# Kernel optimization log

Measured on AMD Instinct MI355X. Metric: run time of the kernel, lower is better.

The kernel has to match this reference:

```python
import jax, jax.numpy as jnp
import numpy as np

B, Nres, TOP_K, NUM_RBF = 2, 2048, 30, 16
MAX_REL = 32  # positional clip range -> 2*32+2 = 66 classes


def _gather_nodes(nodes, idx):
    # nodes: [B, N, ...], idx: [B, N, K] -> [B, N, K, ...]
    return jax.vmap(lambda n, i: n[i])(nodes, idx)


def _rbf(D):
    # D: [..., ] -> [..., NUM_RBF]; mu in [2, 22], sigma = 20/16
    mu = jnp.linspace(2.0, 22.0, NUM_RBF)
    sigma = (22.0 - 2.0) / NUM_RBF
    return jnp.exp(-(((D[..., None] - mu) / sigma) ** 2))


def setup_inputs() -> dict:
    key = jax.random.key(0)
    ks = jax.random.split(key, 4)
    X = jax.random.normal(ks[0], (B, Nres, 4, 3), dtype=jnp.float32) * 3.0
    mask = jnp.ones((B, Nres), dtype=jnp.float32)
    residue_idx = jnp.broadcast_to(jnp.arange(Nres, dtype=jnp.int32)[None], (B, Nres))
    chain_labels = jnp.zeros((B, Nres), dtype=jnp.int32)
    w_pos = jax.random.normal(ks[1], (66, 16), dtype=jnp.float32) * 0.05
    b_pos = jax.random.normal(ks[2], (16,), dtype=jnp.float32) * 0.05
    w_edge = jax.random.normal(ks[3], (416, 128), dtype=jnp.float32) * 0.05
    ln_gamma = jnp.ones((128,), dtype=jnp.float32)
    ln_beta = jnp.zeros((128,), dtype=jnp.float32)
    return dict(X=X, mask=mask, residue_idx=residue_idx, chain_labels=chain_labels,
                w_pos=w_pos, b_pos=b_pos, w_edge=w_edge, ln_gamma=ln_gamma, ln_beta=ln_beta)


def reference(X, mask, residue_idx, chain_labels, w_pos, b_pos, w_edge, ln_gamma, ln_beta):
    # virtual C-beta from N, C, Ca (atom order in X: N=0, C=1, Ca=2, O=3)
    b = X[:, :, 2, :] - X[:, :, 0, :]
    c = X[:, :, 1, :] - X[:, :, 2, :]
    a = jnp.cross(b, c)
    Cb = -0.58273431 * a + 0.56802827 * b - 0.54067466 * c + X[:, :, 2, :]
    N_, C, Ca, O = X[:, :, 0, :], X[:, :, 1, :], X[:, :, 2, :], X[:, :, 3, :]

    # masked kNN on C atoms (ProteinFeatures._dist)
    m2 = mask[:, None, :] * mask[:, :, None]                       # [B,N,N]
    dX = C[:, None, :, :] - C[:, :, None, :]
    D = m2 * jnp.sqrt(jnp.sum(dX ** 2, -1) + 1e-6)
    D_max = jnp.max(D, -1, keepdims=True)
    D_adj = D + (1.0 - m2) * D_max
    neg, E_idx = jax.lax.top_k(-D_adj, TOP_K)                      # smallest-k
    D_neighbors = -neg                                             # [B,N,K]

    # 25-channel RBF features; gather neighbor coords instead of NxN per pair
    atoms = jnp.stack([N_, Ca, Cb, C, O], 0)                       # [5,B,N,3]
    gathered = jax.vmap(lambda A: _gather_nodes(A, E_idx))(atoms)  # [5,B,N,K,3]
    # pair order follows torch source: NN,CaCa,CbCb,CN,CCa,CCb,NCa,NCb,CbCa,
    # NC,CaC,CbC,CaN,CbN,CaCb,OO,CO,OC,NO,ON,CbO,OCa,OCb,CaO  (0=N,1=Ca,2=Cb,3=C,4=O)
    pa = jnp.array([0, 1, 2, 3, 3, 3, 0, 0, 2, 0, 1, 2, 1, 2, 1, 4, 3, 4, 0, 4, 2, 4, 4, 1])
    pb = jnp.array([0, 1, 2, 0, 1, 2, 1, 2, 1, 3, 3, 3, 0, 0, 2, 4, 4, 3, 4, 0, 4, 1, 2, 4])
    A_sel = atoms[pa]                                              # [24,B,N,3]
    Bn_sel = gathered[pb]                                          # [24,B,N,K,3]
    Dp = jnp.sqrt(jnp.sum((A_sel[:, :, :, None, :] - Bn_sel) ** 2, -1) + 1e-6)
    RBF_all = jnp.concatenate([_rbf(D_neighbors)[None], _rbf(Dp)], 0)  # [25,B,N,K,16]
    RBF_all = jnp.moveaxis(RBF_all, 0, 3).reshape(B, Nres, TOP_K, 25 * NUM_RBF)

    # positional encodings over gathered offsets / chain match
    offset = residue_idx[:, :, None] - _gather_nodes(residue_idx, E_idx)   # [B,N,K]
    E_chains = (chain_labels[:, :, None] == _gather_nodes(chain_labels, E_idx)).astype(jnp.int32)
    d = jnp.clip(offset + MAX_REL, 0, 2 * MAX_REL) * E_chains + (1 - E_chains) * (2 * MAX_REL + 1)
    E_pos = w_pos[d] + b_pos                                       # one_hot @ W == gather

    # edge embedding + layernorm
    E = jnp.concatenate([E_pos, RBF_all], -1) @ w_edge             # [B,N,K,128]
    mu = E.mean(-1, keepdims=True)
    var = E.var(-1, keepdims=True)
    E = (E - mu) / jnp.sqrt(var + 1e-5) * ln_gamma + ln_beta
    return E, E_idx
```

## Files before the change

### kernel.cpp

```cpp
#include <hip/hip_runtime.h>
#include <hip/hip_bf16.h>
#include <stdint.h>

#define BB    2
#define NRES  2048
#define TOPK  30
#define NRBF  16
#define NFEAT 416
#define NCH   128
#define NSTR  212
#define NKT   13

typedef __attribute__((ext_vector_type(8))) short bf16x8;
typedef __attribute__((ext_vector_type(4))) float f32x4;

__constant__ int c_pa[24] = {0,1,2,3,3,3,0,0,2,0,1,2,1,2,1,4,3,4,0,4,2,4,4,1};
__constant__ int c_pb[24] = {0,1,2,0,1,2,1,2,1,3,3,3,0,0,2,4,4,3,4,0,4,1,2,4};

static __device__ __forceinline__ unsigned short f2bf(float x) {
  __hip_bfloat16 h = __float2bfloat16(x);
  return *reinterpret_cast<unsigned short*>(&h);
}
static __device__ __forceinline__ unsigned pack2(float lo, float hi) {
  return (unsigned)f2bf(lo) | ((unsigned)f2bf(hi) << 16);
}

__global__ __launch_bounds__(256) void atoms_kernel(const float* __restrict__ X,
                                                    float* __restrict__ atoms,
                                                    float4* __restrict__ Cpk) {
  int id = blockIdx.x * 256 + threadIdx.x;
  if (id >= BB * NRES) return;
  const float* x = X + (size_t)id * 12;
  float nx = x[0], ny = x[1], nz = x[2];
  float cx = x[3], cy = x[4], cz = x[5];
  float ax = x[6], ay = x[7], az = x[8];
  float ox = x[9], oy = x[10], oz = x[11];
  float bx = ax - nx, by = ay - ny, bz = az - nz;
  float ccx = cx - ax, ccy = cy - ay, ccz = cz - az;
  float crx = by * ccz - bz * ccy;
  float cry = bz * ccx - bx * ccz;
  float crz = bx * ccy - by * ccx;
  float cbx = -0.58273431f * crx + 0.56802827f * bx - 0.54067466f * ccx + ax;
  float cby = -0.58273431f * cry + 0.56802827f * by - 0.54067466f * ccy + ay;
  float cbz = -0.58273431f * crz + 0.56802827f * bz - 0.54067466f * ccz + az;
  float* r = atoms + (size_t)id * 16;
  r[0] = nx;  r[1] = ny;  r[2] = nz;
  r[3] = ax;  r[4] = ay;  r[5] = az;
  r[6] = cbx; r[7] = cby; r[8] = cbz;
  r[9] = cx;  r[10] = cy; r[11] = cz;
  r[12] = ox; r[13] = oy; r[14] = oz;
  r[15] = 0.f;
  Cpk[id] = make_float4(cx, cy, cz, 0.f);
}

__global__ __launch_bounds__(256) void wprep_kernel(const float* __restrict__ w_edge,
                                                    unsigned short* __restrict__ wB) {
  int id = blockIdx.x * 256 + threadIdx.x;
  if (id >= NFEAT * NCH) return;
  int j    = id & 7;
  int lane = (id >> 3) & 63;
  int nt   = (id >> 9) & 7;
  int kt   = id >> 12;
  int col  = nt * 16 + (lane & 15);
  int k    = kt * 32 + ((lane >> 4) << 3) + j;
  wB[id] = f2bf(w_edge[(size_t)k * NCH + col]);
}

__global__ __launch_bounds__(256) void topk_kernel(const float4* __restrict__ Cpk,
                                                   int* __restrict__ eidx,
                                                   float* __restrict__ dn,
                                                   float* __restrict__ outI) {
  int tid = threadIdx.x;
  int lane = tid & 63;
  int bi = blockIdx.x * 4 + (tid >> 6);
  int b = bi >> 11;
  int i = bi & (NRES - 1);
  const float4* Cb = Cpk + (size_t)b * NRES;
  float4 ci = Cb[i];

  unsigned long long key[4][8];
  unsigned long long sub[4];
#pragma unroll
  for (int g = 0; g < 4; ++g) {
    sub[g] = ~0ull;
#pragma unroll
    for (int s = 0; s < 8; ++s) {
      int j = lane + 64 * (g * 8 + s);
      float4 cj = Cb[j];
      float dx = cj.x - ci.x, dy = cj.y - ci.y, dz = cj.z - ci.z;
      float sm = __fadd_rn(__fadd_rn(__fadd_rn(__fmul_rn(dx, dx), __fmul_rn(dy, dy)),
                                     __fmul_rn(dz, dz)), 1e-6f);
      float d = sqrtf(sm);
      key[g][s] = ((unsigned long long)__float_as_uint(d) << 32) | (unsigned)j;
      if (key[g][s] < sub[g]) sub[g] = key[g][s];
    }
  }

  for (int k = 0; k < TOPK; ++k) {
    unsigned long long m01 = sub[0] < sub[1] ? sub[0] : sub[1];
    unsigned long long m23 = sub[2] < sub[3] ? sub[2] : sub[3];
    unsigned long long gm = m01 < m23 ? m01 : m23;
#pragma unroll
    for (int off = 32; off; off >>= 1) {
      unsigned long long o = __shfl_xor(gm, off, 64);
      if (o < gm) gm = o;
    }
    if (lane == 0) {
      int idx = (int)(unsigned)(gm & 0xffffffffu);
      eidx[(size_t)bi * TOPK + k] = idx;
      dn[(size_t)bi * TOPK + k] = __uint_as_float((unsigned)(gm >> 32));
      outI[(size_t)bi * TOPK + k] = (float)idx;
    }
#pragma unroll
    for (int g = 0; g < 4; ++g) {
      if (sub[g] == gm) {
        sub[g] = ~0ull;
#pragma unroll
        for (int s = 0; s < 8; ++s) {
          if (key[g][s] == gm) key[g][s] = ~0ull;
          if (key[g][s] < sub[g]) sub[g] = key[g][s];
        }
      }
    }
  }
}

__global__ __launch_bounds__(256) void edge_mfma_kernel(
    const float* __restrict__ atoms, const int* __restrict__ eidx_g,
    const float* __restrict__ dn_g, const int* __restrict__ ridx,
    const int* __restrict__ chain, const float* __restrict__ w_pos,
    const float* __restrict__ b_pos, const unsigned short* __restrict__ wB,
    const float* __restrict__ gamma, const float* __restrict__ beta,
    float* __restrict__ outE) {
  __shared__ __align__(16) unsigned feat[32][NSTR];
  __shared__ float nat[TOPK][16];
  __shared__ float iat[16];
  __shared__ int   eidx_s[TOPK];
  __shared__ float dn_s[TOPK];
  __shared__ int   dsel[TOPK];
  __shared__ float2 lnp[32][4];

  int tid = threadIdx.x;
  int bi = blockIdx.x;
  int b = bi >> 11;

  if (tid < TOPK) {
    eidx_s[tid] = eidx_g[(size_t)bi * TOPK + tid];
    dn_s[tid]   = dn_g[(size_t)bi * TOPK + tid];
  }
  if (tid >= 64 && tid < 80) iat[tid - 64] = atoms[(size_t)bi * 16 + (tid - 64)];
  for (int idx = tid; idx < 2 * NSTR; idx += 256)
    feat[30 + idx / NSTR][idx % NSTR] = 0u;
  __syncthreads();

  for (int idx = tid; idx < TOPK * 16; idx += 256) {
    int e = idx >> 4, f = idx & 15;
    nat[e][f] = atoms[((size_t)(b * NRES) + eidx_s[e]) * 16 + f];
  }
  if (tid < TOPK) {
    int j = eidx_s[tid];
    int off = ridx[bi] - ridx[b * NRES + j];
    int ec = (chain[bi] == chain[b * NRES + j]) ? 1 : 0;
    int d = off + 32; d = d < 0 ? 0 : (d > 64 ? 64 : d);
    dsel[tid] = ec ? d : 65;
  }
  __syncthreads();

  if (tid < TOPK * 8) {
    int e = tid >> 3, p = tid & 7;
    int f0 = p * 2, ds = dsel[e];
    float v0 = w_pos[ds * 16 + f0] + b_pos[f0];
    float v1 = w_pos[ds * 16 + f0 + 1] + b_pos[f0 + 1];
    feat[e][p] = pack2(v0, v1);
  }
  for (int idx = tid; idx < TOPK * 25; idx += 256) {
    int e = idx / 25, g = idx - e * 25;
    float d;
    if (g == 0) {
      d = dn_s[e];
    } else {
      int q = g - 1;
      const float* A  = &iat[c_pa[q] * 3];
      const float* Bv = &nat[e][c_pb[q] * 3];
      float dx = A[0] - Bv[0], dy = A[1] - Bv[1], dz = A[2] - Bv[2];
      d = sqrtf(dx * dx + dy * dy + dz * dz + 1e-6f);
    }
    unsigned* dst = &feat[e][8 + 8 * g];
#pragma unroll
    for (int j = 0; j < 8; ++j) {
      float mu0 = 2.0f + (float)(2 * j) * (20.0f / 15.0f);
      float mu1 = 2.0f + (float)(2 * j + 1) * (20.0f / 15.0f);
      float t0 = (d - mu0) * 0.8f, t1 = (d - mu1) * 0.8f;
      dst[j] = pack2(__expf(-t0 * t0), __expf(-t1 * t1));
    }
  }
  __syncthreads();

  int nq = tid >> 6, lane = tid & 63;
  int q = lane >> 4;
  int ccol = lane & 15;
  const uint4* arow0 = (const uint4*)&feat[ccol][0];
  const uint4* arow1 = (const uint4*)&feat[16 + ccol][0];
  const bf16x8* wBv = (const bf16x8*)wB;

  f32x4 acc00 = {}, acc01 = {}, acc10 = {}, acc11 = {};
#pragma unroll
  for (int kt = 0; kt < NKT; ++kt) {
    union { uint4 u4; bf16x8 v; } a0, a1;
    a0.u4 = arow0[kt * 4 + q];
    a1.u4 = arow1[kt * 4 + q];
    bf16x8 b0 = wBv[(kt * 8 + nq * 2 + 0) * 64 + lane];
    bf16x8 b1 = wBv[(kt * 8 + nq * 2 + 1) * 64 + lane];
    acc00 = __builtin_amdgcn_mfma_f32_16x16x32_bf16(a0.v, b0, acc00, 0, 0, 0);
    acc01 = __builtin_amdgcn_mfma_f32_16x16x32_bf16(a0.v, b1, acc01, 0, 0, 0);
    acc10 = __builtin_amdgcn_mfma_f32_16x16x32_bf16(a1.v, b0, acc10, 0, 0, 0);
    acc11 = __builtin_amdgcn_mfma_f32_16x16x32_bf16(a1.v, b1, acc11, 0, 0, 0);
  }

#pragma unroll
  for (int mh = 0; mh < 2; ++mh) {
#pragma unroll
    for (int reg = 0; reg < 4; ++reg) {
      float v0 = mh ? acc10[reg] : acc00[reg];
      float v1 = mh ? acc11[reg] : acc01[reg];
      float s = v0 + v1, ss = v0 * v0 + v1 * v1;
      s  += __shfl_xor(s, 1, 64);  ss += __shfl_xor(ss, 1, 64);
      s  += __shfl_xor(s, 2, 64);  ss += __shfl_xor(ss, 2, 64);
      s  += __shfl_xor(s, 4, 64);  ss += __shfl_xor(ss, 4, 64);
      s  += __shfl_xor(s, 8, 64);  ss += __shfl_xor(ss, 8, 64);
      if (ccol == 0) lnp[(mh << 4) + q * 4 + reg][nq] = make_float2(s, ss);
    }
  }
  __syncthreads();

  float g0 = gamma[(nq * 2 + 0) * 16 + ccol], be0 = beta[(nq * 2 + 0) * 16 + ccol];
  float g1 = gamma[(nq * 2 + 1) * 16 + ccol], be1 = beta[(nq * 2 + 1) * 16 + ccol];
#pragma unroll
  for (int mh = 0; mh < 2; ++mh) {
#pragma unroll
    for (int reg = 0; reg < 4; ++reg) {
      int m = (mh << 4) + q * 4 + reg;
      if (m < TOPK) {
        float2 p0 = lnp[m][0], p1 = lnp[m][1], p2 = lnp[m][2], p3 = lnp[m][3];
        float s = (p0.x + p1.x) + (p2.x + p3.x);
        float ss = (p0.y + p1.y) + (p2.y + p3.y);
        float mu = s * (1.0f / 128.0f);
        float var = ss * (1.0f / 128.0f) - mu * mu;
        float rstd = rsqrtf(var + 1e-5f);
        float va = mh ? acc10[reg] : acc00[reg];
        float vb = mh ? acc11[reg] : acc01[reg];
        float* o = outE + ((size_t)bi * TOPK + m) * NCH + ccol;
        o[(nq * 2 + 0) * 16] = (va - mu) * rstd * g0 + be0;
        o[(nq * 2 + 1) * 16] = (vb - mu) * rstd * g1 + be1;
      }
    }
  }
}

extern "C" void kernel_launch(void* const* d_in, const int* in_sizes, int n_in,
                              void* d_out, int out_size, void* d_ws, size_t ws_size,
                              hipStream_t stream) {
  const float* X      = (const float*)d_in[0];
  const int*   ridx   = (const int*)d_in[2];
  const int*   chain  = (const int*)d_in[3];
  const float* w_pos  = (const float*)d_in[4];
  const float* b_pos  = (const float*)d_in[5];
  const float* w_edge = (const float*)d_in[6];
  const float* gamma  = (const float*)d_in[7];
  const float* beta   = (const float*)d_in[8];

  float* outE = (float*)d_out;
  float* outI = outE + (size_t)BB * NRES * TOPK * NCH;

  char* p = (char*)d_ws;
  float* atoms = (float*)p;                 p += (size_t)BB * NRES * 16 * 4;
  int*   eidx  = (int*)p;                   p += (size_t)BB * NRES * TOPK * 4;
  float* dn    = (float*)p;                 p += (size_t)BB * NRES * TOPK * 4;
  unsigned short* wB = (unsigned short*)p;  p += (size_t)NCH * NFEAT * 2;
  float4* Cpk  = (float4*)p;

  atoms_kernel<<<(BB * NRES + 255) / 256, 256, 0, stream>>>(X, atoms, Cpk);
  wprep_kernel<<<(NFEAT * NCH + 255) / 256, 256, 0, stream>>>(w_edge, wB);
  topk_kernel<<<BB * NRES / 4, 256, 0, stream>>>(Cpk, eidx, dn, outI);
  edge_mfma_kernel<<<BB * NRES, 256, 0, stream>>>(atoms, eidx, dn, ridx, chain,
                                                  w_pos, b_pos, wB, gamma, beta, outE);
}
```

Baseline: 85.25 us.

## Merge prep kernels, relayout LDS A-tile, prefetch MFMA operands, trim edge-kernel syncs

New measurement: 83.61 us. No clear change (-1.9%).

```diff
diff --git a/kernel.cpp b/kernel.cpp
--- a/kernel.cpp
+++ b/kernel.cpp
@@ -8,7 +8,6 @@
 #define NRBF  16
 #define NFEAT 416
 #define NCH   128
-#define NSTR  212
 #define NKT   13
 
 typedef __attribute__((ext_vector_type(8))) short bf16x8;
@@ -25,45 +24,45 @@
   return (unsigned)f2bf(lo) | ((unsigned)f2bf(hi) << 16);
 }
 
-__global__ __launch_bounds__(256) void atoms_kernel(const float* __restrict__ X,
-                                                    float* __restrict__ atoms,
-                                                    float4* __restrict__ Cpk) {
-  int id = blockIdx.x * 256 + threadIdx.x;
-  if (id >= BB * NRES) return;
-  const float* x = X + (size_t)id * 12;
-  float nx = x[0], ny = x[1], nz = x[2];
-  float cx = x[3], cy = x[4], cz = x[5];
-  float ax = x[6], ay = x[7], az = x[8];
-  float ox = x[9], oy = x[10], oz = x[11];
-  float bx = ax - nx, by = ay - ny, bz = az - nz;
-  float ccx = cx - ax, ccy = cy - ay, ccz = cz - az;
-  float crx = by * ccz - bz * ccy;
-  float cry = bz * ccx - bx * ccz;
-  float crz = bx * ccy - by * ccx;
-  float cbx = -0.58273431f * crx + 0.56802827f * bx - 0.54067466f * ccx + ax;
-  float cby = -0.58273431f * cry + 0.56802827f * by - 0.54067466f * ccy + ay;
-  float cbz = -0.58273431f * crz + 0.56802827f * bz - 0.54067466f * ccz + az;
-  float* r = atoms + (size_t)id * 16;
-  r[0] = nx;  r[1] = ny;  r[2] = nz;
-  r[3] = ax;  r[4] = ay;  r[5] = az;
-  r[6] = cbx; r[7] = cby; r[8] = cbz;
-  r[9] = cx;  r[10] = cy; r[11] = cz;
-  r[12] = ox; r[13] = oy; r[14] = oz;
-  r[15] = 0.f;
-  Cpk[id] = make_float4(cx, cy, cz, 0.f);
-}
-
-__global__ __launch_bounds__(256) void wprep_kernel(const float* __restrict__ w_edge,
-                                                    unsigned short* __restrict__ wB) {
-  int id = blockIdx.x * 256 + threadIdx.x;
-  if (id >= NFEAT * NCH) return;
-  int j    = id & 7;
-  int lane = (id >> 3) & 63;
-  int nt   = (id >> 9) & 7;
-  int kt   = id >> 12;
-  int col  = nt * 16 + (lane & 15);
-  int k    = kt * 32 + ((lane >> 4) << 3) + j;
-  wB[id] = f2bf(w_edge[(size_t)k * NCH + col]);
+__global__ __launch_bounds__(256) void prep_kernel(const float* __restrict__ X,
+                                                   const float* __restrict__ w_edge,
+                                                   float* __restrict__ atoms,
+                                                   float4* __restrict__ Cpk,
+                                                   unsigned short* __restrict__ wB) {
+  if (blockIdx.x < 16) {
+    int id = blockIdx.x * 256 + threadIdx.x;
+    const float* x = X + (size_t)id * 12;
+    float nx = x[0], ny = x[1], nz = x[2];
+    float cx = x[3], cy = x[4], cz = x[5];
+    float ax = x[6], ay = x[7], az = x[8];
+    float ox = x[9], oy = x[10], oz = x[11];
+    float bx = ax - nx, by = ay - ny, bz = az - nz;
+    float ccx = cx - ax, ccy = cy - ay, ccz = cz - az;
+    float crx = by * ccz - bz * ccy;
+    float cry = bz * ccx - bx * ccz;
+    float crz = bx * ccy - by * ccx;
+    float cbx = -0.58273431f * crx + 0.56802827f * bx - 0.54067466f * ccx + ax;
+    float cby = -0.58273431f * cry + 0.56802827f * by - 0.54067466f * ccy + ay;
+    float cbz = -0.58273431f * crz + 0.56802827f * bz - 0.54067466f * ccz + az;
+    float* r = atoms + (size_t)id * 16;
+    r[0] = nx;  r[1] = ny;  r[2] = nz;
+    r[3] = ax;  r[4] = ay;  r[5] = az;
+    r[6] = cbx; r[7] = cby; r[8] = cbz;
+    r[9] = cx;  r[10] = cy; r[11] = cz;
+    r[12] = ox; r[13] = oy; r[14] = oz;
+    r[15] = 0.f;
+    Cpk[id] = make_float4(cx, cy, cz, 0.f);
+  } else {
+    int id = (blockIdx.x - 16) * 256 + threadIdx.x;
+    if (id >= NFEAT * NCH) return;
+    int j    = id & 7;
+    int lane = (id >> 3) & 63;
+    int nt   = (id >> 9) & 7;
+    int kt   = id >> 12;
+    int col  = nt * 16 + (lane & 15);
+    int k    = kt * 32 + ((lane >> 4) << 3) + j;
+    wB[id] = f2bf(w_edge[(size_t)k * NCH + col]);
+  }
 }
 
 __global__ __launch_bounds__(256) void topk_kernel(const float4* __restrict__ Cpk,
@@ -132,10 +131,9 @@
     const float* __restrict__ b_pos, const unsigned short* __restrict__ wB,
     const float* __restrict__ gamma, const float* __restrict__ beta,
     float* __restrict__ outE) {
-  __shared__ __align__(16) unsigned feat[32][NSTR];
+  __shared__ __align__(16) unsigned fa[NKT * 4 * 32 * 4];
   __shared__ float nat[TOPK][16];
   __shared__ float iat[16];
-  __shared__ int   eidx_s[TOPK];
   __shared__ float dn_s[TOPK];
   __shared__ int   dsel[TOPK];
   __shared__ float2 lnp[32][4];
@@ -145,33 +143,31 @@
   int b = bi >> 11;
 
   if (tid < TOPK) {
-    eidx_s[tid] = eidx_g[(size_t)bi * TOPK + tid];
-    dn_s[tid]   = dn_g[(size_t)bi * TOPK + tid];
-  }
-  if (tid >= 64 && tid < 80) iat[tid - 64] = atoms[(size_t)bi * 16 + (tid - 64)];
-  for (int idx = tid; idx < 2 * NSTR; idx += 256)
-    feat[30 + idx / NSTR][idx % NSTR] = 0u;
-  __syncthreads();
-
-  for (int idx = tid; idx < TOPK * 16; idx += 256) {
-    int e = idx >> 4, f = idx & 15;
-    nat[e][f] = atoms[((size_t)(b * NRES) + eidx_s[e]) * 16 + f];
-  }
-  if (tid < TOPK) {
-    int j = eidx_s[tid];
+    dn_s[tid] = dn_g[(size_t)bi * TOPK + tid];
+    int j = eidx_g[(size_t)bi * TOPK + tid];
     int off = ridx[bi] - ridx[b * NRES + j];
     int ec = (chain[bi] == chain[b * NRES + j]) ? 1 : 0;
     int d = off + 32; d = d < 0 ? 0 : (d > 64 ? 64 : d);
     dsel[tid] = ec ? d : 65;
   }
+  if (tid >= 64 && tid < 80) iat[tid - 64] = atoms[(size_t)bi * 16 + (tid - 64)];
+  for (int idx = tid; idx < TOPK * 16; idx += 256) {
+    int e = idx >> 4, f = idx & 15;
+    nat[e][f] = atoms[((size_t)(b * NRES) + eidx_g[(size_t)bi * TOPK + e]) * 16 + f];
+  }
+  for (int idx = tid; idx < NKT * 4 * 2 * 4; idx += 256) {
+    int kt4q = idx >> 3, row = 30 + ((idx >> 2) & 1), jw = idx & 3;
+    fa[(kt4q * 32 + row) * 4 + jw] = 0u;
+  }
   __syncthreads();
 
   if (tid < TOPK * 8) {
-    int e = tid >> 3, p = tid & 7;
-    int f0 = p * 2, ds = dsel[e];
+    int e = tid >> 3, u = tid & 7;
+    int q = u >> 2, jw = u & 3;
+    int f0 = u * 2, ds = dsel[e];
     float v0 = w_pos[ds * 16 + f0] + b_pos[f0];
     float v1 = w_pos[ds * 16 + f0 + 1] + b_pos[f0 + 1];
-    feat[e][p] = pack2(v0, v1);
+    fa[((q * 32) + e) * 4 + jw] = pack2(v0, v1);
   }
   for (int idx = tid; idx < TOPK * 25; idx += 256) {
     int e = idx / 25, g = idx - e * 25;
@@ -179,42 +175,64 @@
     if (g == 0) {
       d = dn_s[e];
     } else {
-      int q = g - 1;
-      const float* A  = &iat[c_pa[q] * 3];
-      const float* Bv = &nat[e][c_pb[q] * 3];
+      int qq = g - 1;
+      const float* A  = &iat[c_pa[qq] * 3];
+      const float* Bv = &nat[e][c_pb[qq] * 3];
       float dx = A[0] - Bv[0], dy = A[1] - Bv[1], dz = A[2] - Bv[2];
       d = sqrtf(dx * dx + dy * dy + dz * dz + 1e-6f);
     }
-    unsigned* dst = &feat[e][8 + 8 * g];
+    unsigned tmp[8];
 #pragma unroll
     for (int j = 0; j < 8; ++j) {
       float mu0 = 2.0f + (float)(2 * j) * (20.0f / 15.0f);
       float mu1 = 2.0f + (float)(2 * j + 1) * (20.0f / 15.0f);
       float t0 = (d - mu0) * 0.8f, t1 = (d - mu1) * 0.8f;
-      dst[j] = pack2(__expf(-t0 * t0), __expf(-t1 * t1));
-    }
+      tmp[j] = pack2(__expf(-t0 * t0), __expf(-t1 * t1));
+    }
+    int u0 = 8 + 8 * g;
+    int kt = u0 >> 4, q0 = (u0 >> 2) & 3;
+    unsigned* dst0 = &fa[(((kt * 4 + q0) * 32) + e) * 4];
+    unsigned* dst1 = &fa[(((kt * 4 + q0 + 1) * 32) + e) * 4];
+    *(uint4*)dst0 = make_uint4(tmp[0], tmp[1], tmp[2], tmp[3]);
+    *(uint4*)dst1 = make_uint4(tmp[4], tmp[5], tmp[6], tmp[7]);
   }
   __syncthreads();
 
   int nq = tid >> 6, lane = tid & 63;
   int q = lane >> 4;
   int ccol = lane & 15;
-  const uint4* arow0 = (const uint4*)&feat[ccol][0];
-  const uint4* arow1 = (const uint4*)&feat[16 + ccol][0];
+  const uint4* faq = ((const uint4*)fa) + q * 32;
   const bf16x8* wBv = (const bf16x8*)wB;
 
+  union AV { uint4 u4; bf16x8 v; };
+  AV a0[2], a1[2];
+  bf16x8 b0[3], b1[3];
+#pragma unroll
+  for (int t = 0; t < 3; ++t) {
+    b0[t] = wBv[((size_t)(t * 8) + nq * 2 + 0) * 64 + lane];
+    b1[t] = wBv[((size_t)(t * 8) + nq * 2 + 1) * 64 + lane];
+  }
+#pragma unroll
+  for (int t = 0; t < 2; ++t) {
+    a0[t].u4 = faq[t * 128 + ccol];
+    a1[t].u4 = faq[t * 128 + 16 + ccol];
+  }
+
   f32x4 acc00 = {}, acc01 = {}, acc10 = {}, acc11 = {};
 #pragma unroll
   for (int kt = 0; kt < NKT; ++kt) {
-    union { uint4 u4; bf16x8 v; } a0, a1;
-    a0.u4 = arow0[kt * 4 + q];
-    a1.u4 = arow1[kt * 4 + q];
-    bf16x8 b0 = wBv[(kt * 8 + nq * 2 + 0) * 64 + lane];
-    bf16x8 b1 = wBv[(kt * 8 + nq * 2 + 1) * 64 + lane];
-    acc00 = __builtin_amdgcn_mfma_f32_16x16x32_bf16(a0.v, b0, acc00, 0, 0, 0);
-    acc01 = __builtin_amdgcn_mfma_f32_16x16x32_bf16(a0.v, b1, acc01, 0, 0, 0);
-    acc10 = __builtin_amdgcn_mfma_f32_16x16x32_bf16(a1.v, b0, acc10, 0, 0, 0);
-    acc11 = __builtin_amdgcn_mfma_f32_16x16x32_bf16(a1.v, b1, acc11, 0, 0, 0);
+    if (kt + 3 < NKT) {
+      b0[(kt + 3) % 3] = wBv[((size_t)((kt + 3) * 8) + nq * 2 + 0) * 64 + lane];
+      b1[(kt + 3) % 3] = wBv[((size_t)((kt + 3) * 8) + nq * 2 + 1) * 64 + lane];
+    }
+    if (kt + 2 < NKT) {
+      a0[(kt + 2) & 1].u4 = faq[(kt + 2) * 128 + ccol];
+      a1[(kt + 2) & 1].u4 = faq[(kt + 2) * 128 + 16 + ccol];
+    }
+    acc00 = __builtin_amdgcn_mfma_f32_16x16x32_bf16(a0[kt & 1].v, b0[kt % 3], acc00, 0, 0, 0);
+    acc01 = __builtin_amdgcn_mfma_f32_16x16x32_bf16(a0[kt & 1].v, b1[kt % 3], acc01, 0, 0, 0);
+    acc10 = __builtin_amdgcn_mfma_f32_16x16x32_bf16(a1[kt & 1].v, b0[kt % 3], acc10, 0, 0, 0);
+    acc11 = __builtin_amdgcn_mfma_f32_16x16x32_bf16(a1[kt & 1].v, b1[kt % 3], acc11, 0, 0, 0);
   }
 
 #pragma unroll
@@ -279,8 +297,7 @@
   unsigned short* wB = (unsigned short*)p;  p += (size_t)NCH * NFEAT * 2;
   float4* Cpk  = (float4*)p;
 
-  atoms_kernel<<<(BB * NRES + 255) / 256, 256, 0, stream>>>(X, atoms, Cpk);
-  wprep_kernel<<<(NFEAT * NCH + 255) / 256, 256, 0, stream>>>(w_edge, wB);
+  prep_kernel<<<16 + (NFEAT * NCH + 255) / 256, 256, 0, stream>>>(X, w_edge, atoms, Cpk, wB);
   topk_kernel<<<BB * NRES / 4, 256, 0, stream>>>(Cpk, eidx, dn, outI);
   edge_mfma_kernel<<<BB * NRES, 256, 0, stream>>>(atoms, eidx, dn, ridx, chain,
                                                   w_pos, b_pos, wB, gamma, beta, outE);
```
